# Performance work log

Hardware: AMD Instinct MI355X
Metric: run time of the kernel (lower is better)

## Reference

```python
import jax, jax.numpy as jnp
import numpy as np

B, T, H, U = 64, 4096, 256, 256


def setup_inputs() -> dict:
    key = jax.random.key(0)
    ks = jax.random.split(key, 8)
    s = 1.0 / np.sqrt(H)
    return {
        "query": jax.random.normal(ks[0], (B, H), dtype=jnp.float32),
        "values": jax.random.normal(ks[1], (B, T, H), dtype=jnp.float32),
        "W1": jax.random.normal(ks[2], (H, U), dtype=jnp.float32) * s,
        "b1": jnp.zeros((U,), dtype=jnp.float32),
        "W2": jax.random.normal(ks[3], (H, U), dtype=jnp.float32) * s,
        "b2": jnp.zeros((U,), dtype=jnp.float32),
        "V": jax.random.normal(ks[4], (U, 1), dtype=jnp.float32) * (1.0 / np.sqrt(U)),
        "bV": jnp.zeros((1,), dtype=jnp.float32),
    }


def reference(query, values, W1, b1, W2, b2, V, bV):
    # query: [B,H] -> [B,1,U]; values: [B,T,H] -> [B,T,U]
    q_proj = (query @ W1 + b1)[:, None, :]            # [B,1,U]
    v_proj = jnp.einsum('bth,hu->btu', values, W2) + b2  # [B,T,U]
    score = jnp.tanh(q_proj + v_proj) @ V + bV        # [B,T,1]
    attention_weights = jax.nn.softmax(score, axis=1)  # softmax over T
    context_vector = jnp.sum(attention_weights * values, axis=1)  # [B,H]
    return context_vector, attention_weights
```

## Files before the change

kernel.cpp:

```cpp
#include <hip/hip_runtime.h>
#include <stdint.h>

#define B_ 64
#define T_ 4096
#define H_ 256
#define U_ 256

typedef float f32x4 __attribute__((ext_vector_type(4)));
typedef short short8 __attribute__((ext_vector_type(8)));

__device__ __forceinline__ short bf16rne(float f) {
    uint32_t x = __builtin_bit_cast(uint32_t, f);
    return (short)((x + 0x7FFFu + ((x >> 16) & 1u)) >> 16);
}

__device__ __forceinline__ float fast_tanh(float x) {
    float e = __expf(2.0f * x);
    return 1.0f - 2.0f * __builtin_amdgcn_rcpf(e + 1.0f);
}

__device__ __forceinline__ void wg_barrier_lds() {
    asm volatile("s_waitcnt lgkmcnt(0)" ::: "memory");
    __builtin_amdgcn_sched_barrier(0);
    __builtin_amdgcn_s_barrier();
    __builtin_amdgcn_sched_barrier(0);
}

__global__ __launch_bounds__(256) void k_prep(const float* __restrict__ W2,
                                              uint16_t* __restrict__ w2t,
                                              const float* __restrict__ query,
                                              const float* __restrict__ W1,
                                              const float* __restrict__ b1,
                                              const float* __restrict__ b2,
                                              float* __restrict__ qpc) {
    if (blockIdx.x < 256) {
        int idx = blockIdx.x * 256 + threadIdx.x;
        int h = idx >> 8;
        int u = idx & 255;
        w2t[u * 256 + h] = (uint16_t)bf16rne(W2[idx]);
    } else {
        __shared__ float qrow[H_];
        int b = blockIdx.x - 256, u = threadIdx.x;
        qrow[u] = query[b * H_ + u];
        __syncthreads();
        float acc = b1[u] + b2[u];
#pragma unroll 8
        for (int h = 0; h < H_; ++h) acc += qrow[h] * W1[h * U_ + u];
        qpc[b * U_ + u] = acc;
    }
}

#define TR 32
#define NT 8
__global__ __launch_bounds__(512, 2) void k_main(const float* __restrict__ values,
                                                 const uint16_t* __restrict__ w2t,
                                                 const float* __restrict__ qpc,
                                                 const float* __restrict__ V,
                                                 float* __restrict__ score,
                                                 float* __restrict__ part_O,
                                                 float* __restrict__ part_s) {
    __shared__ __align__(16) char Ab[TR * 512];
    __shared__ float red[TR][9];
    __shared__ float Ored[TR][16][16];
    __shared__ float sred[TR];

    const int tid = threadIdx.x;
    const int wg = blockIdx.x;
    const int b = wg >> 4;
    const int chunk = (wg & 15) * (NT * TR);

    const int w = tid >> 6;
    const int l = tid & 63;
    const int c = l & 15;
    const int g = l >> 4;

    short8 afr[2][8];
#pragma unroll
    for (int s = 0; s < 2; ++s) {
        const uint16_t* ap = w2t + (size_t)(w * 32 + s * 16 + c) * 256 + g * 8;
#pragma unroll
        for (int ks = 0; ks < 8; ++ks) afr[s][ks] = *(const short8*)(ap + ks * 32);
    }
    float qv[2][4], vv[2][4];
#pragma unroll
    for (int s = 0; s < 2; ++s)
#pragma unroll
        for (int r = 0; r < 4; ++r) {
            int u = w * 32 + s * 16 + g * 4 + r;
            qv[s][r] = qpc[b * U_ + u];
            vv[s][r] = V[u];
        }

    const float* vbase = values + (size_t)b * T_ * H_;
    const int srow = tid >> 4;
    const int q = tid & 15;
    const int sswz = (srow & 7) << 4;
    char* wr0 = Ab + srow * 512 + ((q * 16) ^ sswz);
    char* wr1 = Ab + srow * 512 + ((q * 16 + 256) ^ sswz);
    const float* sbase = vbase + (size_t)srow * H_ + q * 8;

    f32x4 vt0, vt1, vt2, vt3;
    float Oacc[16];
#pragma unroll
    for (int j = 0; j < 16; ++j) Oacc[j] = 0.f;
    float sacc = 0.f;

    {
        const float* nb = sbase + (size_t)chunk * H_;
        vt0 = *(const f32x4*)(nb);       vt1 = *(const f32x4*)(nb + 4);
        vt2 = *(const f32x4*)(nb + 128); vt3 = *(const f32x4*)(nb + 132);
    }

#pragma unroll
    for (int t = 0; t < NT; ++t) {
        wg_barrier_lds();
        {
            short8 s0, s1;
            s0[0] = bf16rne(vt0[0]); s0[1] = bf16rne(vt0[1]);
            s0[2] = bf16rne(vt0[2]); s0[3] = bf16rne(vt0[3]);
            s0[4] = bf16rne(vt1[0]); s0[5] = bf16rne(vt1[1]);
            s0[6] = bf16rne(vt1[2]); s0[7] = bf16rne(vt1[3]);
            s1[0] = bf16rne(vt2[0]); s1[1] = bf16rne(vt2[1]);
            s1[2] = bf16rne(vt2[2]); s1[3] = bf16rne(vt2[3]);
            s1[4] = bf16rne(vt3[0]); s1[5] = bf16rne(vt3[1]);
            s1[6] = bf16rne(vt3[2]); s1[7] = bf16rne(vt3[3]);
            *(short8*)wr0 = s0;
            *(short8*)wr1 = s1;
        }
        if (t > 0) {
            const float* rb = sbase + (size_t)(chunk + (t - 1) * TR) * H_;
            vt0 = *(const f32x4*)(rb);       vt1 = *(const f32x4*)(rb + 4);
            vt2 = *(const f32x4*)(rb + 128); vt3 = *(const f32x4*)(rb + 132);
            float ssum = 0.f;
#pragma unroll
            for (int j = 0; j < 8; ++j) ssum += red[srow][j];
            float wgt = __expf(ssum);
            if (q == 0) {
                sacc += wgt;
                score[(size_t)b * T_ + chunk + (t - 1) * TR + srow] = ssum;
            }
#pragma unroll
            for (int j = 0; j < 4; ++j) {
                Oacc[j]      += wgt * vt0[j];
                Oacc[4 + j]  += wgt * vt1[j];
                Oacc[8 + j]  += wgt * vt2[j];
                Oacc[12 + j] += wgt * vt3[j];
            }
        }
        if (t + 1 < NT) {
            const float* nb = sbase + (size_t)(chunk + (t + 1) * TR) * H_;
            vt0 = *(const f32x4*)(nb);       vt1 = *(const f32x4*)(nb + 4);
            vt2 = *(const f32x4*)(nb + 128); vt3 = *(const f32x4*)(nb + 132);
        }
        wg_barrier_lds();
#pragma unroll
        for (int sub = 0; sub < 2; ++sub) {
            const char* rp = Ab + (sub * 16 + c) * 512;
            const int swz = (c & 7) << 4;
            f32x4 acc0 = (f32x4)(0.0f);
            f32x4 acc1 = (f32x4)(0.0f);
#pragma unroll
            for (int ks = 0; ks < 8; ++ks) {
                short8 bf = *(const short8*)(rp + ((ks * 64 + g * 16) ^ swz));
                acc0 = __builtin_amdgcn_mfma_f32_16x16x32_bf16(afr[0][ks], bf, acc0, 0, 0, 0);
                acc1 = __builtin_amdgcn_mfma_f32_16x16x32_bf16(afr[1][ks], bf, acc1, 0, 0, 0);
            }
            float p = 0.f;
#pragma unroll
            for (int r = 0; r < 4; ++r) {
                p += fast_tanh(acc0[r] + qv[0][r]) * vv[0][r];
                p += fast_tanh(acc1[r] + qv[1][r]) * vv[1][r];
            }
            p += __shfl_xor(p, 16, 64);
            p += __shfl_xor(p, 32, 64);
            if (g == 0) red[sub * 16 + c][w] = p;
        }
    }
    __syncthreads();
    {
        const float* rb = sbase + (size_t)(chunk + (NT - 1) * TR) * H_;
        vt0 = *(const f32x4*)(rb);       vt1 = *(const f32x4*)(rb + 4);
        vt2 = *(const f32x4*)(rb + 128); vt3 = *(const f32x4*)(rb + 132);
        float ssum = 0.f;
#pragma unroll
        for (int j = 0; j < 8; ++j) ssum += red[srow][j];
        float wgt = __expf(ssum);
        if (q == 0) {
            sacc += wgt;
            score[(size_t)b * T_ + chunk + (NT - 1) * TR + srow] = ssum;
        }
#pragma unroll
        for (int j = 0; j < 4; ++j) {
            Oacc[j]      += wgt * vt0[j];
            Oacc[4 + j]  += wgt * vt1[j];
            Oacc[8 + j]  += wgt * vt2[j];
            Oacc[12 + j] += wgt * vt3[j];
        }
    }
#pragma unroll
    for (int j = 0; j < 16; ++j) Ored[srow][q][j] = Oacc[j];
    if (q == 0) sred[srow] = sacc;
    __syncthreads();
    if (tid < 256) {
        int col = tid;
        int qq, jj;
        if (col < 128) { qq = col >> 3; jj = col & 7; }
        else           { qq = (col - 128) >> 3; jj = 8 + (col & 7); }
        float o = 0.f;
#pragma unroll
        for (int s = 0; s < TR; ++s) o += Ored[s][qq][jj];
        part_O[(size_t)wg * 256 + col] = o;
    }
    if (tid == 0) {
        float sb = 0.f;
#pragma unroll
        for (int s = 0; s < TR; ++s) sb += sred[s];
        part_s[wg] = sb;
    }
}

__global__ __launch_bounds__(256) void k_fin(const float* __restrict__ part_O,
                                             const float* __restrict__ part_s,
                                             const float* __restrict__ score,
                                             float* __restrict__ ctx,
                                             float* __restrict__ weights) {
    int b = blockIdx.x >> 3;
    int j = blockIdx.x & 7;
    int col = threadIdx.x;
    float sb = 0.f;
#pragma unroll
    for (int ch = 0; ch < 16; ++ch) sb += part_s[b * 16 + ch];
    float inv = 1.0f / sb;
    if (j == 0) {
        float o = 0.f;
#pragma unroll
        for (int ch = 0; ch < 16; ++ch) o += part_O[(size_t)(b * 16 + ch) * 256 + col];
        ctx[b * H_ + col] = o * inv;
    }
#pragma unroll
    for (int i = 0; i < 2; ++i) {
        int idx = j * 512 + i * 256 + col;
        float s = score[(size_t)b * T_ + idx];
        weights[(size_t)b * T_ + idx] = __expf(s) * inv;
    }
}

extern "C" void kernel_launch(void* const* d_in, const int* in_sizes, int n_in,
                              void* d_out, int out_size, void* d_ws, size_t ws_size,
                              hipStream_t stream) {
    const float* query  = (const float*)d_in[0];
    const float* values = (const float*)d_in[1];
    const float* W1     = (const float*)d_in[2];
    const float* b1     = (const float*)d_in[3];
    const float* W2     = (const float*)d_in[4];
    const float* b2     = (const float*)d_in[5];
    const float* V      = (const float*)d_in[6];

    float* out = (float*)d_out;
    float* ctx = out;
    float* weights = out + B_ * H_;

    char* ws = (char*)d_ws;
    uint16_t* w2t   = (uint16_t*)ws;
    float* qpc      = (float*)(ws + 131072);
    float* scorebuf = (float*)(ws + 131072 + 65536);
    float* part_O   = (float*)(ws + 131072 + 65536 + 1048576);
    float* part_s   = (float*)(ws + 131072 + 65536 + 2097152);

    k_prep<<<dim3(320), dim3(256), 0, stream>>>(W2, w2t, query, W1, b1, b2, qpc);
    k_main<<<dim3(1024), dim3(512), 0, stream>>>(values, w2t, qpc, V, scorebuf,
                                                 part_O, part_s);
    k_fin<<<dim3(512), dim3(256), 0, stream>>>(part_O, part_s, scorebuf, ctx, weights);
}
```

Before: 92.65 us.

## Double-buffer LDS tiles to drop one barrier per iteration and use packed bf16 conversion

Splits the bf16 values tile and the score reduction buffer into two LDS slots, so the MFMA score computation for tile t runs while tile t+1 is written into the other slot. This removes one of the two workgroup barriers per loop iteration. The scalar bf16 rounding is replaced by the hardware v_cvt_pk_bf16_f32 instruction, and the reduction reads become vectorized f32x4 loads from padded rows. The cost is double the LDS use, which could lower occupancy, and a prefetch distance that now depends on the new ordering of global loads.

```diff
diff --git a/kernel.cpp b/kernel.cpp
--- a/kernel.cpp
+++ b/kernel.cpp
@@ -8,6 +8,7 @@
 
 typedef float f32x4 __attribute__((ext_vector_type(4)));
 typedef short short8 __attribute__((ext_vector_type(8)));
+typedef unsigned int uint4v __attribute__((ext_vector_type(4)));
 
 __device__ __forceinline__ short bf16rne(float f) {
     uint32_t x = __builtin_bit_cast(uint32_t, f);
@@ -24,6 +25,16 @@
     __builtin_amdgcn_sched_barrier(0);
     __builtin_amdgcn_s_barrier();
     __builtin_amdgcn_sched_barrier(0);
+}
+
+__device__ __forceinline__ uint4v pack_bf16x8(const f32x4 a, const f32x4 b) {
+    uint32_t w0, w1, w2, w3;
+    asm("v_cvt_pk_bf16_f32 %0, %1, %2" : "=v"(w0) : "v"(a[0]), "v"(a[1]));
+    asm("v_cvt_pk_bf16_f32 %0, %1, %2" : "=v"(w1) : "v"(a[2]), "v"(a[3]));
+    asm("v_cvt_pk_bf16_f32 %0, %1, %2" : "=v"(w2) : "v"(b[0]), "v"(b[1]));
+    asm("v_cvt_pk_bf16_f32 %0, %1, %2" : "=v"(w3) : "v"(b[2]), "v"(b[3]));
+    uint4v r; r[0] = w0; r[1] = w1; r[2] = w2; r[3] = w3;
+    return r;
 }
 
 __global__ __launch_bounds__(256) void k_prep(const float* __restrict__ W2,
@@ -59,8 +70,8 @@
                                                  float* __restrict__ score,
                                                  float* __restrict__ part_O,
                                                  float* __restrict__ part_s) {
-    __shared__ __align__(16) char Ab[TR * 512];
-    __shared__ float red[TR][9];
+    __shared__ __align__(16) char Ab[2][TR * 512];
+    __shared__ __align__(16) float red[2][TR][12];
     __shared__ float Ored[TR][16][16];
     __shared__ float sred[TR];
 
@@ -95,8 +106,8 @@
     const int srow = tid >> 4;
     const int q = tid & 15;
     const int sswz = (srow & 7) << 4;
-    char* wr0 = Ab + srow * 512 + ((q * 16) ^ sswz);
-    char* wr1 = Ab + srow * 512 + ((q * 16 + 256) ^ sswz);
+    const int wroff = srow * 512 + ((q * 16) ^ sswz);
+
     const float* sbase = vbase + (size_t)srow * H_ + q * 8;
 
     f32x4 vt0, vt1, vt2, vt3;
@@ -109,31 +120,55 @@
         const float* nb = sbase + (size_t)chunk * H_;
         vt0 = *(const f32x4*)(nb);       vt1 = *(const f32x4*)(nb + 4);
         vt2 = *(const f32x4*)(nb + 128); vt3 = *(const f32x4*)(nb + 132);
+        *(uint4v*)(Ab[0] + wroff)       = pack_bf16x8(vt0, vt1);
+        *(uint4v*)(Ab[0] + wroff + 256) = pack_bf16x8(vt2, vt3);
+        const float* nb1 = sbase + (size_t)(chunk + TR) * H_;
+        vt0 = *(const f32x4*)(nb1);       vt1 = *(const f32x4*)(nb1 + 4);
+        vt2 = *(const f32x4*)(nb1 + 128); vt3 = *(const f32x4*)(nb1 + 132);
     }
 
 #pragma unroll
     for (int t = 0; t < NT; ++t) {
         wg_barrier_lds();
-        {
-            short8 s0, s1;
-            s0[0] = bf16rne(vt0[0]); s0[1] = bf16rne(vt0[1]);
-            s0[2] = bf16rne(vt0[2]); s0[3] = bf16rne(vt0[3]);
-            s0[4] = bf16rne(vt1[0]); s0[5] = bf16rne(vt1[1]);
-            s0[6] = bf16rne(vt1[2]); s0[7] = bf16rne(vt1[3]);
-            s1[0] = bf16rne(vt2[0]); s1[1] = bf16rne(vt2[1]);
-            s1[2] = bf16rne(vt2[2]); s1[3] = bf16rne(vt2[3]);
-            s1[4] = bf16rne(vt3[0]); s1[5] = bf16rne(vt3[1]);
-            s1[6] = bf16rne(vt3[2]); s1[7] = bf16rne(vt3[3]);
-            *(short8*)wr0 = s0;
-            *(short8*)wr1 = s1;
-        }
+
+#pragma unroll
+        for (int sub = 0; sub < 2; ++sub) {
+            const char* rp = Ab[t & 1] + (sub * 16 + c) * 512;
+            const int swz = (c & 7) << 4;
+            f32x4 acc0 = (f32x4)(0.0f);
+            f32x4 acc1 = (f32x4)(0.0f);
+#pragma unroll
+            for (int ks = 0; ks < 8; ++ks) {
+                short8 bf = *(const short8*)(rp + ((ks * 64 + g * 16) ^ swz));
+                acc0 = __builtin_amdgcn_mfma_f32_16x16x32_bf16(afr[0][ks], bf, acc0, 0, 0, 0);
+                acc1 = __builtin_amdgcn_mfma_f32_16x16x32_bf16(afr[1][ks], bf, acc1, 0, 0, 0);
+            }
+            float p = 0.f;
+#pragma unroll
+            for (int r = 0; r < 4; ++r) {
+                p += fast_tanh(acc0[r] + qv[0][r]) * vv[0][r];
+                p += fast_tanh(acc1[r] + qv[1][r]) * vv[1][r];
+            }
+            p += __shfl_xor(p, 16, 64);
+            p += __shfl_xor(p, 32, 64);
+            if (g == 0) red[t & 1][sub * 16 + c][w] = p;
+        }
+
+        if (t + 1 < NT) {
+            char* dst = Ab[(t + 1) & 1] + wroff;
+            *(uint4v*)(dst)       = pack_bf16x8(vt0, vt1);
+            *(uint4v*)(dst + 256) = pack_bf16x8(vt2, vt3);
+        }
+
         if (t > 0) {
             const float* rb = sbase + (size_t)(chunk + (t - 1) * TR) * H_;
             vt0 = *(const f32x4*)(rb);       vt1 = *(const f32x4*)(rb + 4);
             vt2 = *(const f32x4*)(rb + 128); vt3 = *(const f32x4*)(rb + 132);
-            float ssum = 0.f;
-#pragma unroll
-            for (int j = 0; j < 8; ++j) ssum += red[srow][j];
+            const float* rr = &red[(t - 1) & 1][srow][0];
+            f32x4 r0 = *(const f32x4*)(rr);
+            f32x4 r1 = *(const f32x4*)(rr + 4);
+            float ssum = ((r0[0] + r0[1]) + (r0[2] + r0[3])) +
+                         ((r1[0] + r1[1]) + (r1[2] + r1[3]));
             float wgt = __expf(ssum);
             if (q == 0) {
                 sacc += wgt;
@@ -147,33 +182,11 @@
                 Oacc[12 + j] += wgt * vt3[j];
             }
         }
-        if (t + 1 < NT) {
-            const float* nb = sbase + (size_t)(chunk + (t + 1) * TR) * H_;
+
+        if (t + 2 < NT) {
+            const float* nb = sbase + (size_t)(chunk + (t + 2) * TR) * H_;
             vt0 = *(const f32x4*)(nb);       vt1 = *(const f32x4*)(nb + 4);
             vt2 = *(const f32x4*)(nb + 128); vt3 = *(const f32x4*)(nb + 132);
-        }
-        wg_barrier_lds();
-#pragma unroll
-        for (int sub = 0; sub < 2; ++sub) {
-            const char* rp = Ab + (sub * 16 + c) * 512;
-            const int swz = (c & 7) << 4;
-            f32x4 acc0 = (f32x4)(0.0f);
-            f32x4 acc1 = (f32x4)(0.0f);
-#pragma unroll
-            for (int ks = 0; ks < 8; ++ks) {
-                short8 bf = *(const short8*)(rp + ((ks * 64 + g * 16) ^ swz));
-                acc0 = __builtin_amdgcn_mfma_f32_16x16x32_bf16(afr[0][ks], bf, acc0, 0, 0, 0);
-                acc1 = __builtin_amdgcn_mfma_f32_16x16x32_bf16(afr[1][ks], bf, acc1, 0, 0, 0);
-            }
-            float p = 0.f;
-#pragma unroll
-            for (int r = 0; r < 4; ++r) {
-                p += fast_tanh(acc0[r] + qv[0][r]) * vv[0][r];
-                p += fast_tanh(acc1[r] + qv[1][r]) * vv[1][r];
-            }
-            p += __shfl_xor(p, 16, 64);
-            p += __shfl_xor(p, 32, 64);
-            if (g == 0) red[sub * 16 + c][w] = p;
         }
     }
     __syncthreads();
@@ -181,9 +194,11 @@
         const float* rb = sbase + (size_t)(chunk + (NT - 1) * TR) * H_;
         vt0 = *(const f32x4*)(rb);       vt1 = *(const f32x4*)(rb + 4);
         vt2 = *(const f32x4*)(rb + 128); vt3 = *(const f32x4*)(rb + 132);
-        float ssum = 0.f;
-#pragma unroll
-        for (int j = 0; j < 8; ++j) ssum += red[srow][j];
+        const float* rr = &red[(NT - 1) & 1][srow][0];
+        f32x4 r0 = *(const f32x4*)(rr);
+        f32x4 r1 = *(const f32x4*)(rr + 4);
+        float ssum = ((r0[0] + r0[1]) + (r0[2] + r0[3])) +
+                     ((r1[0] + r1[1]) + (r1[2] + r1[3]));
         float wgt = __expf(ssum);
         if (q == 0) {
             sacc += wgt;
```

After: 101.7 us. 1.1x slower.
